# Optimization experiments

Hardware: AMD Instinct MI355X
Metric: run time of the kernel (lower is better)

## Reference

```python
import jax, jax.numpy as jnp
import numpy as np

B, N, C, M = 2, 16384, 256, 16  # M = win_w*win_h for stage 1
W = N // M

def setup_inputs() -> dict:
    key = jax.random.key(0)
    ks = jax.random.split(key, 8)
    s = 1.0 / np.sqrt(C)
    return {
        "input": jax.random.normal(ks[0], (B, N, C), jnp.float32),
        "embed_qk": jax.random.normal(ks[1], (B, W, M, M, 3), jnp.float32),
        "Wq": jax.random.normal(ks[2], (C, C), jnp.float32) * s,
        "bq": jax.random.normal(ks[3], (C,), jnp.float32) * 0.01,
        "Wk": jax.random.normal(ks[4], (C, C), jnp.float32) * s,
        "bk": jax.random.normal(ks[5], (C,), jnp.float32) * 0.01,
        "Wp": jax.random.normal(ks[6], (3, 1), jnp.float32) * 0.5,
        "bp": jax.random.normal(ks[7], (1,), jnp.float32) * 0.01,
    }

def reference(input, embed_qk, Wq, bq, Wk, bk, Wp, bp):
    WIN = 16  # stage==1 -> win_w*win_h = 4*4
    b, n, c = input.shape
    add = (-n) % WIN
    q = jax.nn.elu(input @ Wq + bq) + 1.0
    k = jax.nn.elu(input @ Wk + bk) + 1.0
    v = input
    pad = ((0, 0), (0, add), (0, 0))
    q_win = jnp.pad(q, pad).reshape(b, -1, WIN, c)
    k_win = jnp.pad(k, pad).reshape(b, -1, WIN, c)
    v_win = jnp.pad(v, pad).reshape(b, -1, WIN, c)
    # second ELU+1 feature map (as in the original)
    phi_q = jax.nn.elu(q_win) + 1.0
    phi_k = jax.nn.elu(k_win) + 1.0
    # KV sums over ALL windows w -> (b, m, c, d)
    KV = jnp.einsum('bwmc,bwmd->bmcd', phi_k, v_win)
    # (b, w, n, m, d) expanded intermediate
    att = jnp.einsum('bwnc,bmcd->bwnmd', phi_q, KV)
    p = (embed_qk @ Wp + bp)[..., 0]  # (b, w, m, m)
    att = att + p[..., None]
    out = att.reshape(b, -1, c)[:, :n, :]
    return out
```

## Files before the change

### kernel.cpp

```cpp
#include <hip/hip_runtime.h>

typedef __attribute__((ext_vector_type(8))) short s16x8;
typedef __attribute__((ext_vector_type(8))) ushort u16x8;
typedef __attribute__((ext_vector_type(4))) ushort u16x4;
typedef __attribute__((ext_vector_type(4))) float f32x4v;

namespace {

constexpr int kB = 2;
constexpr int kN = 16384;
constexpr int kC = 256;

__device__ __forceinline__ ushort f2bf(float f) {
  union { float f; uint u; } v; v.f = f;
  uint u = v.u + 0x7fffu + ((v.u >> 16) & 1u);
  return (ushort)(u >> 16);
}

__device__ __forceinline__ float phi_act(float x) {
  return x > 0.f ? x + 2.f : __expf(x) + 1.f;
}

template <int FM, int FN>
__device__ __forceinline__ void wave_mma(const ushort* __restrict__ A,
                                         const ushort* __restrict__ B, int ar0,
                                         int bc0, int lane,
                                         f32x4v acc[FM][FN]) {
  const int lo = lane & 15, hi = lane >> 4;
  s16x8 a[FM], b[FN];
#pragma unroll
  for (int i = 0; i < FM; ++i) {
    int r = ar0 + i * 16 + lo;
    a[i] = *reinterpret_cast<const s16x8*>(A + r * 32 + ((hi ^ ((r >> 1) & 3)) << 3));
  }
#pragma unroll
  for (int j = 0; j < FN; ++j) {
    int c = bc0 + j * 16 + lo;
    b[j] = *reinterpret_cast<const s16x8*>(B + c * 32 + ((hi ^ ((c >> 1) & 3)) << 3));
  }
#pragma unroll
  for (int i = 0; i < FM; ++i)
#pragma unroll
    for (int j = 0; j < FN; ++j)
      acc[i][j] = __builtin_amdgcn_mfma_f32_16x16x32_bf16(a[i], b[j], acc[i][j], 0, 0, 0);
}

__global__ __launch_bounds__(256) void wt_kernel(const float* __restrict__ Wq,
                                                 const float* __restrict__ Wk,
                                                 ushort* __restrict__ WqT,
                                                 ushort* __restrict__ WkT) {
  __shared__ float ts[64][65];
  const float* W = blockIdx.z ? Wk : Wq;
  ushort* WT = blockIdx.z ? WkT : WqT;
  const int bi = blockIdx.x, bj = blockIdx.y, t = threadIdx.x;
  for (int rep = 0; rep < 16; ++rep) {
    int e = rep * 256 + t, r = e >> 6, c = e & 63;
    ts[r][c] = W[(size_t)(bi * 64 + r) * kC + bj * 64 + c];
  }
  __syncthreads();
  for (int rep = 0; rep < 16; ++rep) {
    int e = rep * 256 + t, j = e >> 6, k = e & 63;
    WT[(size_t)(bj * 64 + j) * kC + bi * 64 + k] = f2bf(ts[k][j]);
  }
}

__global__ __launch_bounds__(256) void regroup_kernel(const float* __restrict__ X,
                                                      ushort* __restrict__ G) {
  __shared__ ushort ls[64 * 288];
  const int cb = blockIdx.x;
  const int wb = blockIdx.y;
  const int b = blockIdx.z;
  const int t = threadIdx.x;
  const float* src = X + ((size_t)b * kN + wb * 1024) * kC + cb * 16;
  const int lr = t >> 2, cg = t & 3;
  for (int rep = 0; rep < 16; ++rep) {
    int row = rep * 64 + lr;
    float4 v = *reinterpret_cast<const float4*>(src + (size_t)row * kC + cg * 4);
    int w = row >> 4, m = row & 15;
    int base = w * 288 + m * 18 + cg * 4;
    uint p0 = (uint)f2bf(v.x) | ((uint)f2bf(v.y) << 16);
    uint p1 = (uint)f2bf(v.z) | ((uint)f2bf(v.w) << 16);
    *reinterpret_cast<uint*>(ls + base) = p0;
    *reinterpret_cast<uint*>(ls + base + 2) = p1;
  }
  __syncthreads();
  const int m = t >> 4, c_l = t & 15;
  const size_t gbase = ((size_t)b * 16 + m) * 128 + wb * 8;
#pragma unroll
  for (int r = 0; r < 8; ++r) {
    u16x8 v;
#pragma unroll
    for (int wl = 0; wl < 8; ++wl) v[wl] = ls[(r * 8 + wl) * 288 + m * 18 + c_l];
    *reinterpret_cast<u16x8*>(G + (gbase + r) * 2048 + (size_t)(cb * 16 + c_l) * 8) = v;
  }
}

template <bool GROUPED, int RPB>
__global__ __launch_bounds__(256) void proj_kernel(const float* __restrict__ X,
                                                   const ushort* __restrict__ WT,
                                                   const float* __restrict__ bias,
                                                   ushort* __restrict__ Outp) {
  __shared__ __align__(16) ushort smem[16384];
  ushort* Alds = smem;
  ushort* Blds = smem + 4096;
  const int t = threadIdx.x, lane = t & 63, wv = t >> 6;
  const int gr0 = blockIdx.x * 128, jb = blockIdx.y, j0 = jb * 128;
  const int b = gr0 / RPB, n0 = gr0 % RPB;
  const float* Asrc = X + ((size_t)b * kN + n0) * kC;
  const ushort* Bsrc = WT + (size_t)j0 * kC;
  const int ar = t >> 2, aj = t & 3;

  float4 a0[2], a1[2];
  u16x8 rb[2];
  auto loadT = [&](int k0) {
    a0[0] = *reinterpret_cast<const float4*>(Asrc + (size_t)ar * kC + k0 + aj * 8);
    a1[0] = *reinterpret_cast<const float4*>(Asrc + (size_t)ar * kC + k0 + aj * 8 + 4);
    a0[1] = *reinterpret_cast<const float4*>(Asrc + (size_t)(ar + 64) * kC + k0 + aj * 8);
    a1[1] = *reinterpret_cast<const float4*>(Asrc + (size_t)(ar + 64) * kC + k0 + aj * 8 + 4);
    rb[0] = *reinterpret_cast<const u16x8*>(Bsrc + (size_t)ar * kC + k0 + aj * 8);
    rb[1] = *reinterpret_cast<const u16x8*>(Bsrc + (size_t)(ar + 64) * kC + k0 + aj * 8);
  };
  auto writeT = [&]() {
#pragma unroll
    for (int k = 0; k < 2; ++k) {
      int row = ar + 64 * k;
      int ch = aj ^ ((row >> 1) & 3);
      u16x8 v;
      v[0] = f2bf(a0[k].x); v[1] = f2bf(a0[k].y); v[2] = f2bf(a0[k].z); v[3] = f2bf(a0[k].w);
      v[4] = f2bf(a1[k].x); v[5] = f2bf(a1[k].y); v[6] = f2bf(a1[k].z); v[7] = f2bf(a1[k].w);
      *reinterpret_cast<u16x8*>(Alds + row * 32 + ch * 8) = v;
      *reinterpret_cast<u16x8*>(Blds + row * 32 + ch * 8) = rb[k];
    }
  };

  f32x4v acc[4][4] = {};
  const int wr0 = (wv >> 1) * 64, wc0 = (wv & 1) * 64;
  loadT(0);
  for (int ks = 0; ks < 8; ++ks) {
    __syncthreads();
    writeT();
    if (ks < 7) loadT((ks + 1) * 32);
    __syncthreads();
    wave_mma<4, 4>(Alds, Blds, wr0, wc0, lane, acc);
  }

  const int lo = lane & 15, hi = lane >> 4;
  float bv[4];
#pragma unroll
  for (int fj = 0; fj < 4; ++fj) bv[fj] = bias[j0 + wc0 + fj * 16 + lo];

  if (GROUPED) {
    __syncthreads();
#pragma unroll
    for (int fi = 0; fi < 4; ++fi)
#pragma unroll
      for (int fj = 0; fj < 4; ++fj)
#pragma unroll
        for (int r = 0; r < 4; ++r) {
          int row = wr0 + fi * 16 + hi * 4 + r;
          int col = wc0 + fj * 16 + lo;
          smem[row * 128 + col] = f2bf(phi_act(acc[fi][fj][r] + bv[fj]));
        }
    __syncthreads();
    const int wblk = n0 >> 7;
    const int mh = t >> 7, c_l = t & 127;
#pragma unroll
    for (int rep = 0; rep < 8; ++rep) {
      int m = mh * 8 + rep;
      u16x8 v;
#pragma unroll
      for (int wl = 0; wl < 8; ++wl) v[wl] = smem[(wl * 16 + m) * 128 + c_l];
      *reinterpret_cast<u16x8*>(Outp + ((((size_t)b * 16 + m) * 128 + wblk) * 256 + j0 + c_l) * 8) = v;
    }
  } else {
#pragma unroll
    for (int fi = 0; fi < 4; ++fi)
#pragma unroll
      for (int fj = 0; fj < 4; ++fj)
#pragma unroll
        for (int r = 0; r < 4; ++r) {
          int row = gr0 + wr0 + fi * 16 + hi * 4 + r;
          int col = j0 + wc0 + fj * 16 + lo;
          Outp[(size_t)row * kC + col] = f2bf(phi_act(acc[fi][fj][r] + bv[fj]));
        }
  }
}

__global__ __launch_bounds__(256) void kv_kernel(const ushort* __restrict__ Kg,
                                                 const ushort* __restrict__ Vg,
                                                 ushort* __restrict__ KVT) {
  __shared__ __align__(16) ushort smem[6144];
  ushort* Alds = smem;
  ushort* Blds = smem + 4096;
  const int t = threadIdx.x, lane = t & 63, wv = t >> 6;
  const int cb = blockIdx.x, db = blockIdx.y, bm = blockIdx.z;
  const ushort* Abase = Kg + (size_t)bm * 262144 + (size_t)(cb * 128) * 8;
  const ushort* Bbase = Vg + (size_t)bm * 262144 + (size_t)(db * 64) * 8;
  const int ac = t & 127, ajh = t >> 7;
  const int bd = t & 63, bj = t >> 6;

  u16x8 ra[2], rbv;
  auto loadT = [&](int s) {
    int w4 = s * 4;
    ra[0] = *reinterpret_cast<const u16x8*>(Abase + ((size_t)(w4 + ajh) * 256 + ac) * 8);
    ra[1] = *reinterpret_cast<const u16x8*>(Abase + ((size_t)(w4 + ajh + 2) * 256 + ac) * 8);
    rbv = *reinterpret_cast<const u16x8*>(Bbase + ((size_t)(w4 + bj) * 256 + bd) * 8);
  };
  auto writeT = [&]() {
    int sw = (ac >> 1) & 3;
    *reinterpret_cast<u16x8*>(Alds + ac * 32 + ((ajh ^ sw) << 3)) = ra[0];
    *reinterpret_cast<u16x8*>(Alds + ac * 32 + (((ajh + 2) ^ sw) << 3)) = ra[1];
    *reinterpret_cast<u16x8*>(Blds + bd * 32 + ((bj ^ ((bd >> 1) & 3)) << 3)) = rbv;
  };

  f32x4v acc[4][2] = {};
  const int wr0 = (wv >> 1) * 64, wc0 = (wv & 1) * 32;
  loadT(0);
  for (int s = 0; s < 32; ++s) {
    __syncthreads();
    writeT();
    if (s < 31) loadT(s + 1);
    __syncthreads();
    wave_mma<4, 2>(Alds, Blds, wr0, wc0, lane, acc);
  }
  const int lo = lane & 15, hi = lane >> 4;
#pragma unroll
  for (int fi = 0; fi < 4; ++fi)
#pragma unroll
    for (int fj = 0; fj < 2; ++fj) {
      int d = db * 64 + wc0 + fj * 16 + lo;
      int c = cb * 128 + wr0 + fi * 16 + hi * 4;
      u16x4 v = {f2bf(acc[fi][fj][0]), f2bf(acc[fi][fj][1]),
                 f2bf(acc[fi][fj][2]), f2bf(acc[fi][fj][3])};
      *reinterpret_cast<u16x4*>(KVT + ((size_t)bm * 256 + d) * 256 + c) = v;
    }
}

__global__ __launch_bounds__(256) void out_kernel(const ushort* __restrict__ Q,
                                                  const ushort* __restrict__ KVT,
                                                  const float* __restrict__ EQK,
                                                  const float* __restrict__ Wp,
                                                  const float* __restrict__ bp,
                                                  float* __restrict__ Out) {
  __shared__ __align__(16) ushort smem[8192];
  __shared__ float Ps[128];
  ushort* Alds = smem;
  ushort* Blds = smem + 4096;
  const int t = threadIdx.x, lane = t & 63, wv = t >> 6;
  const int qb = blockIdx.x, db = blockIdx.y, bm = blockIdx.z;
  const int b = bm >> 4, m = bm & 15;
  if (t < 128) {
    int qr = qb * 128 + t;
    const float* e = EQK + (((size_t)(b * 1024 + (qr >> 4)) * 16 + (qr & 15)) * 16 + m) * 3;
    Ps[t] = e[0] * Wp[0] + e[1] * Wp[1] + e[2] * Wp[2] + bp[0];
  }
  const ushort* Asrc = Q + ((size_t)b * 1024 + qb * 128) * kC;
  const ushort* Bsrc = KVT + (size_t)bm * 65536 + (size_t)db * 128 * kC;
  const int ar = t >> 2, aj = t & 3;

  u16x8 rga[2], rgb[2];
  auto loadT = [&](int k0) {
    rga[0] = *reinterpret_cast<const u16x8*>(Asrc + (size_t)ar * kC + k0 + aj * 8);
    rga[1] = *reinterpret_cast<const u16x8*>(Asrc + (size_t)(ar + 64) * kC + k0 + aj * 8);
    rgb[0] = *reinterpret_cast<const u16x8*>(Bsrc + (size_t)ar * kC + k0 + aj * 8);
    rgb[1] = *reinterpret_cast<const u16x8*>(Bsrc + (size_t)(ar + 64) * kC + k0 + aj * 8);
  };
  auto writeT = [&]() {
#pragma unroll
    for (int k = 0; k < 2; ++k) {
      int row = ar + 64 * k;
      int ch = aj ^ ((row >> 1) & 3);
      *reinterpret_cast<u16x8*>(Alds + row * 32 + ch * 8) = rga[k];
      *reinterpret_cast<u16x8*>(Blds + row * 32 + ch * 8) = rgb[k];
    }
  };

  f32x4v acc[4][4] = {};
  const int wr0 = (wv >> 1) * 64, wc0 = (wv & 1) * 64;
  loadT(0);
  for (int ks = 0; ks < 8; ++ks) {
    __syncthreads();
    writeT();
    if (ks < 7) loadT((ks + 1) * 32);
    __syncthreads();
    wave_mma<4, 4>(Alds, Blds, wr0, wc0, lane, acc);
  }
  const int lo = lane & 15, hi = lane >> 4;
#pragma unroll
  for (int fi = 0; fi < 4; ++fi)
#pragma unroll
    for (int r = 0; r < 4; ++r) {
      int rowl = wr0 + fi * 16 + hi * 4 + r;
      int qr = qb * 128 + rowl;
      float p = Ps[rowl];
      size_t orow = ((size_t)b * kN + (size_t)qr * 16 + m) * kC;
#pragma unroll
      for (int fj = 0; fj < 4; ++fj) {
        int d = db * 128 + wc0 + fj * 16 + lo;
        Out[orow + d] = acc[fi][fj][r] + p;
      }
    }
}

}

extern "C" void kernel_launch(void* const* d_in, const int* in_sizes, int n_in,
                              void* d_out, int out_size, void* d_ws,
                              size_t ws_size, hipStream_t stream) {
  const float* input = (const float*)d_in[0];
  const float* eqk = (const float*)d_in[1];
  const float* Wq = (const float*)d_in[2];
  const float* bq = (const float*)d_in[3];
  const float* Wk = (const float*)d_in[4];
  const float* bk = (const float*)d_in[5];
  const float* Wp = (const float*)d_in[6];
  const float* bp = (const float*)d_in[7];
  float* out = (float*)d_out;

  ushort* ws = (ushort*)d_ws;
  ushort* WqT = ws;
  ushort* WkT = WqT + 65536;
  ushort* xg = WkT + 65536;
  ushort* kg = xg + 8388608;
  ushort* qf = kg + 8388608;
  ushort* kvt = qf + 524288;

  wt_kernel<<<dim3(4, 4, 2), 256, 0, stream>>>(Wq, Wk, WqT, WkT);
  regroup_kernel<<<dim3(16, 16, 2), 256, 0, stream>>>(input, xg);
  proj_kernel<true, 16384><<<dim3(256, 2), 256, 0, stream>>>(input, WkT, bk, kg);
  proj_kernel<false, 1024><<<dim3(16, 2), 256, 0, stream>>>(input, WqT, bq, qf);
  kv_kernel<<<dim3(2, 4, 32), 256, 0, stream>>>(kg, xg, kvt);
  out_kernel<<<dim3(8, 2, 32), 256, 0, stream>>>(qf, kvt, eqk, Wp, bp, out);
}
```

Baseline: 163.8 us.

## Merge Q/K projections into one launch and load MFMA operands directly from global

The separate K and Q projection launches become a single 544-block launch. Each projection block now stages its full 128x256 bf16 weight slice in LDS once and reads the fp32 activations straight from global into MFMA registers, instead of staging both through double-buffered LDS with two barriers per k-step. The kv and out kernels likewise drop LDS staging, load MFMA fragments directly from global, use a 1D grid with a swizzled block order to improve L2 locality, and kv uses smaller 64x64 tiles for more blocks. This removes barrier and LDS-copy overhead and one launch, at the cost of less coalesced global fragment loads and relying on cache hits.

```diff
diff --git a/kernel.cpp b/kernel.cpp
--- a/kernel.cpp
+++ b/kernel.cpp
@@ -10,6 +10,7 @@
 constexpr int kB = 2;
 constexpr int kN = 16384;
 constexpr int kC = 256;
+constexpr int kQR = 1024;
 
 __device__ __forceinline__ ushort f2bf(float f) {
   union { float f; uint u; } v; v.f = f;
@@ -19,30 +20,6 @@
 
 __device__ __forceinline__ float phi_act(float x) {
   return x > 0.f ? x + 2.f : __expf(x) + 1.f;
-}
-
-template <int FM, int FN>
-__device__ __forceinline__ void wave_mma(const ushort* __restrict__ A,
-                                         const ushort* __restrict__ B, int ar0,
-                                         int bc0, int lane,
-                                         f32x4v acc[FM][FN]) {
-  const int lo = lane & 15, hi = lane >> 4;
-  s16x8 a[FM], b[FN];
-#pragma unroll
-  for (int i = 0; i < FM; ++i) {
-    int r = ar0 + i * 16 + lo;
-    a[i] = *reinterpret_cast<const s16x8*>(A + r * 32 + ((hi ^ ((r >> 1) & 3)) << 3));
-  }
-#pragma unroll
-  for (int j = 0; j < FN; ++j) {
-    int c = bc0 + j * 16 + lo;
-    b[j] = *reinterpret_cast<const s16x8*>(B + c * 32 + ((hi ^ ((c >> 1) & 3)) << 3));
-  }
-#pragma unroll
-  for (int i = 0; i < FM; ++i)
-#pragma unroll
-    for (int j = 0; j < FN; ++j)
-      acc[i][j] = __builtin_amdgcn_mfma_f32_16x16x32_bf16(a[i], b[j], acc[i][j], 0, 0, 0);
 }
 
 __global__ __launch_bounds__(256) void wt_kernel(const float* __restrict__ Wq,
@@ -95,62 +72,77 @@
   }
 }
 
-template <bool GROUPED, int RPB>
-__global__ __launch_bounds__(256) void proj_kernel(const float* __restrict__ X,
-                                                   const ushort* __restrict__ WT,
-                                                   const float* __restrict__ bias,
-                                                   ushort* __restrict__ Outp) {
-  __shared__ __align__(16) ushort smem[16384];
-  ushort* Alds = smem;
-  ushort* Blds = smem + 4096;
+__global__ __launch_bounds__(256) void proj_kernel(
+    const float* __restrict__ X, const ushort* __restrict__ WqT,
+    const ushort* __restrict__ WkT, const float* __restrict__ bq,
+    const float* __restrict__ bk, ushort* __restrict__ kg,
+    ushort* __restrict__ qf) {
+  __shared__ __align__(16) ushort smem[32768];
+
   const int t = threadIdx.x, lane = t & 63, wv = t >> 6;
-  const int gr0 = blockIdx.x * 128, jb = blockIdx.y, j0 = jb * 128;
-  const int b = gr0 / RPB, n0 = gr0 % RPB;
-  const float* Asrc = X + ((size_t)b * kN + n0) * kC;
-  const ushort* Bsrc = WT + (size_t)j0 * kC;
-  const int ar = t >> 2, aj = t & 3;
-
-  float4 a0[2], a1[2];
-  u16x8 rb[2];
-  auto loadT = [&](int k0) {
-    a0[0] = *reinterpret_cast<const float4*>(Asrc + (size_t)ar * kC + k0 + aj * 8);
-    a1[0] = *reinterpret_cast<const float4*>(Asrc + (size_t)ar * kC + k0 + aj * 8 + 4);
-    a0[1] = *reinterpret_cast<const float4*>(Asrc + (size_t)(ar + 64) * kC + k0 + aj * 8);
-    a1[1] = *reinterpret_cast<const float4*>(Asrc + (size_t)(ar + 64) * kC + k0 + aj * 8 + 4);
-    rb[0] = *reinterpret_cast<const u16x8*>(Bsrc + (size_t)ar * kC + k0 + aj * 8);
-    rb[1] = *reinterpret_cast<const u16x8*>(Bsrc + (size_t)(ar + 64) * kC + k0 + aj * 8);
-  };
-  auto writeT = [&]() {
-#pragma unroll
-    for (int k = 0; k < 2; ++k) {
-      int row = ar + 64 * k;
-      int ch = aj ^ ((row >> 1) & 3);
-      u16x8 v;
-      v[0] = f2bf(a0[k].x); v[1] = f2bf(a0[k].y); v[2] = f2bf(a0[k].z); v[3] = f2bf(a0[k].w);
-      v[4] = f2bf(a1[k].x); v[5] = f2bf(a1[k].y); v[6] = f2bf(a1[k].z); v[7] = f2bf(a1[k].w);
-      *reinterpret_cast<u16x8*>(Alds + row * 32 + ch * 8) = v;
-      *reinterpret_cast<u16x8*>(Blds + row * 32 + ch * 8) = rb[k];
-    }
-  };
-
+  const int bx = blockIdx.x;
+  const bool kmode = bx < 512;
+  int b, n0, jb;
+  const ushort* WT;
+  const float* bias;
+  if (kmode) {
+    int rt = bx >> 1; jb = bx & 1; b = rt >> 7; n0 = (rt & 127) * 128;
+    WT = WkT; bias = bk;
+  } else {
+    int i = bx - 512; int rt = i >> 1; jb = i & 1; b = rt >> 3; n0 = (rt & 7) * 128;
+    WT = WqT; bias = bq;
+  }
+  const int j0 = jb * 128;
+  const float* Xbase = X + ((size_t)b * kN + n0) * kC;
+
+  for (int rep = 0; rep < 16; ++rep) {
+    int idx = rep * 256 + t;
+    int jj = idx >> 5, cc = idx & 31;
+    u16x8 v = *reinterpret_cast<const u16x8*>(WT + (size_t)(j0 + jj) * kC + cc * 8);
+    *reinterpret_cast<u16x8*>(smem + jj * 256 + ((cc ^ (jj & 31)) << 3)) = v;
+  }
+  __syncthreads();
+
+  const int lo = lane & 15, hi = lane >> 4;
+  const int wr0 = (wv >> 1) * 64, wc0 = (wv & 1) * 64;
   f32x4v acc[4][4] = {};
-  const int wr0 = (wv >> 1) * 64, wc0 = (wv & 1) * 64;
-  loadT(0);
-  for (int ks = 0; ks < 8; ++ks) {
+
+#pragma unroll 2
+  for (int s = 0; s < 8; ++s) {
+    s16x8 a[4], bf[4];
+#pragma unroll
+    for (int fi = 0; fi < 4; ++fi) {
+      const float* ap = Xbase + (size_t)(wr0 + fi * 16 + lo) * kC + s * 32 + hi * 8;
+      float4 f0 = *reinterpret_cast<const float4*>(ap);
+      float4 f1 = *reinterpret_cast<const float4*>(ap + 4);
+      s16x8 av;
+      av[0] = (short)f2bf(f0.x); av[1] = (short)f2bf(f0.y);
+      av[2] = (short)f2bf(f0.z); av[3] = (short)f2bf(f0.w);
+      av[4] = (short)f2bf(f1.x); av[5] = (short)f2bf(f1.y);
+      av[6] = (short)f2bf(f1.z); av[7] = (short)f2bf(f1.w);
+      a[fi] = av;
+    }
+#pragma unroll
+    for (int fj = 0; fj < 4; ++fj) {
+      int jl = wc0 + fj * 16 + lo;
+      bf[fj] = *reinterpret_cast<const s16x8*>(
+          smem + jl * 256 + (((s * 4 + hi) ^ (jl & 31)) << 3));
+    }
+#pragma unroll
+    for (int fi = 0; fi < 4; ++fi)
+#pragma unroll
+      for (int fj = 0; fj < 4; ++fj)
+        acc[fi][fj] = __builtin_amdgcn_mfma_f32_16x16x32_bf16(a[fi], bf[fj], acc[fi][fj], 0, 0, 0);
+  }
+
+  float bv[4];
+#pragma unroll
+  for (int fj = 0; fj < 4; ++fj) bv[fj] = bias[j0 + wc0 + fj * 16 + lo];
+
+  if (kmode) {
+    const int wgrp = (bx >> 1) & 127;
     __syncthreads();
-    writeT();
-    if (ks < 7) loadT((ks + 1) * 32);
-    __syncthreads();
-    wave_mma<4, 4>(Alds, Blds, wr0, wc0, lane, acc);
-  }
-
-  const int lo = lane & 15, hi = lane >> 4;
-  float bv[4];
-#pragma unroll
-  for (int fj = 0; fj < 4; ++fj) bv[fj] = bias[j0 + wc0 + fj * 16 + lo];
-
-  if (GROUPED) {
-    __syncthreads();
+    ushort* ep = smem;
 #pragma unroll
     for (int fi = 0; fi < 4; ++fi)
 #pragma unroll
@@ -159,18 +151,18 @@
         for (int r = 0; r < 4; ++r) {
           int row = wr0 + fi * 16 + hi * 4 + r;
           int col = wc0 + fj * 16 + lo;
-          smem[row * 128 + col] = f2bf(phi_act(acc[fi][fj][r] + bv[fj]));
+          ep[row * 128 + col] = f2bf(phi_act(acc[fi][fj][r] + bv[fj]));
         }
     __syncthreads();
-    const int wblk = n0 >> 7;
-    const int mh = t >> 7, c_l = t & 127;
+    const int m = t >> 4, cl = t & 15;
 #pragma unroll
     for (int rep = 0; rep < 8; ++rep) {
-      int m = mh * 8 + rep;
+      int c = rep * 16 + cl;
       u16x8 v;
 #pragma unroll
-      for (int wl = 0; wl < 8; ++wl) v[wl] = smem[(wl * 16 + m) * 128 + c_l];
-      *reinterpret_cast<u16x8*>(Outp + ((((size_t)b * 16 + m) * 128 + wblk) * 256 + j0 + c_l) * 8) = v;
+      for (int wl = 0; wl < 8; ++wl) v[wl] = ep[(wl * 16 + m) * 128 + c];
+      *reinterpret_cast<u16x8*>(
+          kg + (((size_t)(b * 16 + m) * 128 + wgrp) * 256 + j0 + c) * 8) = v;
     }
   } else {
 #pragma unroll
@@ -179,113 +171,89 @@
       for (int fj = 0; fj < 4; ++fj)
 #pragma unroll
         for (int r = 0; r < 4; ++r) {
-          int row = gr0 + wr0 + fi * 16 + hi * 4 + r;
+          int row = n0 + wr0 + fi * 16 + hi * 4 + r;
           int col = j0 + wc0 + fj * 16 + lo;
-          Outp[(size_t)row * kC + col] = f2bf(phi_act(acc[fi][fj][r] + bv[fj]));
+          qf[((size_t)b * kQR + row) * kC + col] = f2bf(phi_act(acc[fi][fj][r] + bv[fj]));
         }
   }
 }
 
-__global__ __launch_bounds__(256) void kv_kernel(const ushort* __restrict__ Kg,
-                                                 const ushort* __restrict__ Vg,
-                                                 ushort* __restrict__ KVT) {
-  __shared__ __align__(16) ushort smem[6144];
-  ushort* Alds = smem;
-  ushort* Blds = smem + 4096;
+__global__ __launch_bounds__(256) void kv_kernel(const ushort* __restrict__ kg,
+                                                 const ushort* __restrict__ xg,
+                                                 ushort* __restrict__ kvt) {
   const int t = threadIdx.x, lane = t & 63, wv = t >> 6;
-  const int cb = blockIdx.x, db = blockIdx.y, bm = blockIdx.z;
-  const ushort* Abase = Kg + (size_t)bm * 262144 + (size_t)(cb * 128) * 8;
-  const ushort* Bbase = Vg + (size_t)bm * 262144 + (size_t)(db * 64) * 8;
-  const int ac = t & 127, ajh = t >> 7;
-  const int bd = t & 63, bj = t >> 6;
-
-  u16x8 ra[2], rbv;
-  auto loadT = [&](int s) {
-    int w4 = s * 4;
-    ra[0] = *reinterpret_cast<const u16x8*>(Abase + ((size_t)(w4 + ajh) * 256 + ac) * 8);
-    ra[1] = *reinterpret_cast<const u16x8*>(Abase + ((size_t)(w4 + ajh + 2) * 256 + ac) * 8);
-    rbv = *reinterpret_cast<const u16x8*>(Bbase + ((size_t)(w4 + bj) * 256 + bd) * 8);
-  };
-  auto writeT = [&]() {
-    int sw = (ac >> 1) & 3;
-    *reinterpret_cast<u16x8*>(Alds + ac * 32 + ((ajh ^ sw) << 3)) = ra[0];
-    *reinterpret_cast<u16x8*>(Alds + ac * 32 + (((ajh + 2) ^ sw) << 3)) = ra[1];
-    *reinterpret_cast<u16x8*>(Blds + bd * 32 + ((bj ^ ((bd >> 1) & 3)) << 3)) = rbv;
-  };
-
-  f32x4v acc[4][2] = {};
-  const int wr0 = (wv >> 1) * 64, wc0 = (wv & 1) * 32;
-  loadT(0);
+  const int swz = (blockIdx.x & 7) * 64 + (blockIdx.x >> 3);
+  const int bm = swz >> 4, cb = swz & 3, db = (swz >> 2) & 3;
+  const int lo = lane & 15, hi = lane >> 4;
+  const int c0 = cb * 64 + (wv >> 1) * 32;
+  const int d0 = db * 64 + (wv & 1) * 32;
+  const ushort* Ab = kg + (size_t)bm * 262144;
+  const ushort* Bb = xg + (size_t)bm * 262144;
+
+  f32x4v acc[2][2] = {};
+#pragma unroll 4
   for (int s = 0; s < 32; ++s) {
-    __syncthreads();
-    writeT();
-    if (s < 31) loadT(s + 1);
-    __syncthreads();
-    wave_mma<4, 2>(Alds, Blds, wr0, wc0, lane, acc);
-  }
-  const int lo = lane & 15, hi = lane >> 4;
-#pragma unroll
-  for (int fi = 0; fi < 4; ++fi)
+    const int wg = s * 4 + hi;
+    s16x8 a0 = *reinterpret_cast<const s16x8*>(Ab + ((size_t)wg * 256 + c0 + lo) * 8);
+    s16x8 a1 = *reinterpret_cast<const s16x8*>(Ab + ((size_t)wg * 256 + c0 + 16 + lo) * 8);
+    s16x8 b0 = *reinterpret_cast<const s16x8*>(Bb + ((size_t)wg * 256 + d0 + lo) * 8);
+    s16x8 b1 = *reinterpret_cast<const s16x8*>(Bb + ((size_t)wg * 256 + d0 + 16 + lo) * 8);
+    acc[0][0] = __builtin_amdgcn_mfma_f32_16x16x32_bf16(a0, b0, acc[0][0], 0, 0, 0);
+    acc[0][1] = __builtin_amdgcn_mfma_f32_16x16x32_bf16(a0, b1, acc[0][1], 0, 0, 0);
+    acc[1][0] = __builtin_amdgcn_mfma_f32_16x16x32_bf16(a1, b0, acc[1][0], 0, 0, 0);
+    acc[1][1] = __builtin_amdgcn_mfma_f32_16x16x32_bf16(a1, b1, acc[1][1], 0, 0, 0);
+  }
+#pragma unroll
+  for (int fi = 0; fi < 2; ++fi)
 #pragma unroll
     for (int fj = 0; fj < 2; ++fj) {
-      int d = db * 64 + wc0 + fj * 16 + lo;
-      int c = cb * 128 + wr0 + fi * 16 + hi * 4;
+      int d = d0 + fj * 16 + lo;
+      int c = c0 + fi * 16 + hi * 4;
       u16x4 v = {f2bf(acc[fi][fj][0]), f2bf(acc[fi][fj][1]),
                  f2bf(acc[fi][fj][2]), f2bf(acc[fi][fj][3])};
-      *reinterpret_cast<u16x4*>(KVT + ((size_t)bm * 256 + d) * 256 + c) = v;
-    }
-}
-
-__global__ __launch_bounds__(256) void out_kernel(const ushort* __restrict__ Q,
-                                                  const ushort* __restrict__ KVT,
-                                                  const float* __restrict__ EQK,
-                                                  const float* __restrict__ Wp,
-                                                  const float* __restrict__ bp,
-                                                  float* __restrict__ Out) {
-  __shared__ __align__(16) ushort smem[8192];
+      *reinterpret_cast<u16x4*>(kvt + ((size_t)bm * 256 + d) * 256 + c) = v;
+    }
+}
+
+__global__ __launch_bounds__(256) void out_kernel(
+    const ushort* __restrict__ qf, const ushort* __restrict__ kvt,
+    const float* __restrict__ EQK, const float* __restrict__ Wp,
+    const float* __restrict__ bp, float* __restrict__ Out) {
   __shared__ float Ps[128];
-  ushort* Alds = smem;
-  ushort* Blds = smem + 4096;
   const int t = threadIdx.x, lane = t & 63, wv = t >> 6;
-  const int qb = blockIdx.x, db = blockIdx.y, bm = blockIdx.z;
-  const int b = bm >> 4, m = bm & 15;
+  const int swz = (blockIdx.x & 7) * 64 + (blockIdx.x >> 3);
+  const int bm = swz >> 4, qb = swz & 7, db = (swz >> 3) & 1;
+  const int b = bm >> 4, mm = bm & 15;
   if (t < 128) {
     int qr = qb * 128 + t;
-    const float* e = EQK + (((size_t)(b * 1024 + (qr >> 4)) * 16 + (qr & 15)) * 16 + m) * 3;
+    const float* e = EQK + (((size_t)(b * 1024 + (qr >> 4)) * 16 + (qr & 15)) * 16 + mm) * 3;
     Ps[t] = e[0] * Wp[0] + e[1] * Wp[1] + e[2] * Wp[2] + bp[0];
   }
-  const ushort* Asrc = Q + ((size_t)b * 1024 + qb * 128) * kC;
-  const ushort* Bsrc = KVT + (size_t)bm * 65536 + (size_t)db * 128 * kC;
-  const int ar = t >> 2, aj = t & 3;
-
-  u16x8 rga[2], rgb[2];
-  auto loadT = [&](int k0) {
-    rga[0] = *reinterpret_cast<const u16x8*>(Asrc + (size_t)ar * kC + k0 + aj * 8);
-    rga[1] = *reinterpret_cast<const u16x8*>(Asrc + (size_t)(ar + 64) * kC + k0 + aj * 8);
-    rgb[0] = *reinterpret_cast<const u16x8*>(Bsrc + (size_t)ar * kC + k0 + aj * 8);
-    rgb[1] = *reinterpret_cast<const u16x8*>(Bsrc + (size_t)(ar + 64) * kC + k0 + aj * 8);
-  };
-  auto writeT = [&]() {
-#pragma unroll
-    for (int k = 0; k < 2; ++k) {
-      int row = ar + 64 * k;
-      int ch = aj ^ ((row >> 1) & 3);
-      *reinterpret_cast<u16x8*>(Alds + row * 32 + ch * 8) = rga[k];
-      *reinterpret_cast<u16x8*>(Blds + row * 32 + ch * 8) = rgb[k];
-    }
-  };
+  __syncthreads();
+
+  const int lo = lane & 15, hi = lane >> 4;
+  const int wr0 = (wv >> 1) * 64, wc0 = (wv & 1) * 64;
+  const ushort* Aq = qf + ((size_t)b * kQR + qb * 128) * kC;
+  const ushort* Bk = kvt + ((size_t)bm * 256 + db * 128) * kC;
 
   f32x4v acc[4][4] = {};
-  const int wr0 = (wv >> 1) * 64, wc0 = (wv & 1) * 64;
-  loadT(0);
-  for (int ks = 0; ks < 8; ++ks) {
-    __syncthreads();
-    writeT();
-    if (ks < 7) loadT((ks + 1) * 32);
-    __syncthreads();
-    wave_mma<4, 4>(Alds, Blds, wr0, wc0, lane, acc);
-  }
-  const int lo = lane & 15, hi = lane >> 4;
+#pragma unroll 2
+  for (int s = 0; s < 8; ++s) {
+    s16x8 a[4], bf[4];
+#pragma unroll
+    for (int fi = 0; fi < 4; ++fi)
+      a[fi] = *reinterpret_cast<const s16x8*>(
+          Aq + (size_t)(wr0 + fi * 16 + lo) * kC + s * 32 + hi * 8);
+#pragma unroll
+    for (int fj = 0; fj < 4; ++fj)
+      bf[fj] = *reinterpret_cast<const s16x8*>(
+          Bk + (size_t)(wc0 + fj * 16 + lo) * kC + s * 32 + hi * 8);
+#pragma unroll
+    for (int fi = 0; fi < 4; ++fi)
+#pragma unroll
+      for (int fj = 0; fj < 4; ++fj)
+        acc[fi][fj] = __builtin_amdgcn_mfma_f32_16x16x32_bf16(a[fi], bf[fj], acc[fi][fj], 0, 0, 0);
+  }
 #pragma unroll
   for (int fi = 0; fi < 4; ++fi)
 #pragma unroll
@@ -293,7 +261,7 @@
       int rowl = wr0 + fi * 16 + hi * 4 + r;
       int qr = qb * 128 + rowl;
       float p = Ps[rowl];
-      size_t orow = ((size_t)b * kN + (size_t)qr * 16 + m) * kC;
+      size_t orow = ((size_t)b * kN + (size_t)qr * 16 + mm) * kC;
 #pragma unroll
       for (int fj = 0; fj < 4; ++fj) {
         int d = db * 128 + wc0 + fj * 16 + lo;
@@ -327,8 +295,7 @@
 
   wt_kernel<<<dim3(4, 4, 2), 256, 0, stream>>>(Wq, Wk, WqT, WkT);
   regroup_kernel<<<dim3(16, 16, 2), 256, 0, stream>>>(input, xg);
-  proj_kernel<true, 16384><<<dim3(256, 2), 256, 0, stream>>>(input, WkT, bk, kg);
-  proj_kernel<false, 1024><<<dim3(16, 2), 256, 0, stream>>>(input, WqT, bq, qf);
-  kv_kernel<<<dim3(2, 4, 32), 256, 0, stream>>>(kg, xg, kvt);
-  out_kernel<<<dim3(8, 2, 32), 256, 0, stream>>>(qf, kvt, eqk, Wp, bp, out);
-}
+  proj_kernel<<<dim3(544), 256, 0, stream>>>(input, WqT, WkT, bq, bk, kg, qf);
+  kv_kernel<<<dim3(512), 256, 0, stream>>>(kg, xg, kvt);
+  out_kernel<<<dim3(512), 256, 0, stream>>>(qf, kvt, eqk, Wp, bp, out);
+}
```

Result: slower. 173.0 us (+5.7%).
